# Kernel optimization log

Hardware: AMD Instinct MI355X
Metric: run time of the kernel (lower is better)

## Reference

```python
import jax, jax.numpy as jnp
import numpy as np

N = 100000   # nodes
R = 4        # relations
E = 200000   # edges per relation
IN = 256
HID = 64
OUT = 64
H = 8        # heads
NEG_SLOPE = 0.2


def setup_inputs() -> dict:
    key = jax.random.key(0)
    ks = jax.random.split(key, 13)
    s = 0.05
    return {
        "x": jax.random.normal(ks[0], (N, IN), jnp.float32),
        "src": jax.random.randint(ks[1], (R, E), 0, N),
        "dst": jax.random.randint(ks[2], (R, E), 0, N),
        "W0": jax.random.normal(ks[3], (R, IN, H * HID), jnp.float32) * s,
        "al0": jax.random.normal(ks[4], (R, H, HID), jnp.float32) * s,
        "ar0": jax.random.normal(ks[5], (R, H, HID), jnp.float32) * s,
        "W1": jax.random.normal(ks[6], (R, H * HID, H * HID), jnp.float32) * s,
        "al1": jax.random.normal(ks[7], (R, H, HID), jnp.float32) * s,
        "ar1": jax.random.normal(ks[8], (R, H, HID), jnp.float32) * s,
        "W2": jax.random.normal(ks[9], (R, H * HID, H * OUT), jnp.float32) * s,
        "al2": jax.random.normal(ks[10], (R, H, OUT), jnp.float32) * s,
        "ar2": jax.random.normal(ks[11], (R, H, OUT), jnp.float32) * s,
    }


def gat_layer(h, src, dst, W, al, ar):
    """Multi-relation GATConv layer; HeteroGraphConv sums ELU'd per-relation outputs.
    h: [N, in]; W: [R, in, H*O]; al/ar: [R, H, O]. Returns [N, H, O]."""
    n = h.shape[0]
    nheads, odim = al.shape[1], al.shape[2]
    acc = jnp.zeros((n, nheads, odim), h.dtype)
    for r in range(W.shape[0]):  # small fixed relation count
        f = (h @ W[r]).reshape(n, nheads, odim)          # [N,H,O]
        el = jnp.sum(f * al[r], axis=-1)                  # [N,H]
        er = jnp.sum(f * ar[r], axis=-1)                  # [N,H]
        s_r, d_r = src[r], dst[r]
        e = jax.nn.leaky_relu(el[s_r] + er[d_r], NEG_SLOPE)  # [E,H]
        # segment softmax over incoming edges per destination node
        m = jax.ops.segment_max(e, d_r, num_segments=n)
        m = jnp.where(jnp.isfinite(m), m, 0.0)
        ex = jnp.exp(e - m[d_r])
        denom = jax.ops.segment_sum(ex, d_r, num_segments=n)
        alpha = ex / (denom[d_r] + 1e-9)                  # [E,H]
        msg = f[s_r] * alpha[:, :, None]                  # [E,H,O]
        out_r = jax.ops.segment_sum(msg, d_r, num_segments=n)  # [N,H,O]
        acc = acc + jax.nn.elu(out_r)
    return acc


def reference(x, src, dst, W0, al0, ar0, W1, al1, ar1, W2, al2, ar2):
    h = gat_layer(x, src, dst, W0, al0, ar0).reshape(N, -1)   # flatten heads
    h = gat_layer(h, src, dst, W1, al1, ar1).reshape(N, -1)   # flatten heads
    h = gat_layer(h, src, dst, W2, al2, ar2).mean(axis=1)     # mean over heads
    return h
```

## Files before the change

### kernel.cpp

```cpp
#include <hip/hip_runtime.h>
#include <hip/hip_bf16.h>
#include <math.h>

#define NNODES 100000
#define NREL 4
#define NEDGE 200000
#define NH 8
#define FDIM 512
#define NMB 782

typedef float f4 __attribute__((ext_vector_type(4)));
typedef __bf16 bf16x8 __attribute__((ext_vector_type(8)));
typedef __bf16 bf16x4 __attribute__((ext_vector_type(4)));

__device__ __forceinline__ float eluf(float v) { return v > 0.f ? v : expm1f(v); }
__device__ __forceinline__ void gload16(const __bf16* g, __bf16* l) {
  __builtin_amdgcn_global_load_lds((const __attribute__((address_space(1))) void*)g,
                                   (__attribute__((address_space(3))) void*)l, 16, 0, 0);
}

__global__ void k_conv(const float* __restrict__ in, __bf16* __restrict__ outp) {
  int i = (blockIdx.x * 256 + threadIdx.x) * 4;
  f4 v = *(const f4*)(in + i);
  bf16x4 o = {(__bf16)v.x, (__bf16)v.y, (__bf16)v.z, (__bf16)v.w};
  *(bf16x4*)(outp + i) = o;
}
__global__ void k_copyb(const __bf16* __restrict__ in, __bf16* __restrict__ outp) {
  int i = (blockIdx.x * 256 + threadIdx.x) * 8;
  *(bf16x8*)(outp + i) = *(const bf16x8*)(in + i);
}

__global__ void k_transW(const float* __restrict__ W, __bf16* __restrict__ Wt, int K) {
  __shared__ float tile[32][33];
  int r = blockIdx.z;
  const float* Wr = W + (size_t)r * K * FDIM;
  __bf16* Wtr = Wt + (size_t)r * FDIM * K;
  int k0 = blockIdx.x * 32, n0 = blockIdx.y * 32;
  int tx = threadIdx.x, ty = threadIdx.y;
  for (int i = ty; i < 32; i += 8)
    tile[i][tx] = Wr[(size_t)(k0 + i) * FDIM + n0 + tx];
  __syncthreads();
  for (int i = ty; i < 32; i += 8)
    Wtr[(size_t)(n0 + i) * K + k0 + tx] = (__bf16)tile[tx][i];
}

__global__ __launch_bounds__(256) void k_gemm(const __bf16* __restrict__ A,
                                              const __bf16* __restrict__ BT,
                                              __bf16* __restrict__ C,
                                              const float* __restrict__ al,
                                              const float* __restrict__ ar,
                                              float* __restrict__ el,
                                              float* __restrict__ er, int M, int K,
                                              int nb4shift, int cpx) {
  __shared__ alignas(16) __bf16 lA[3][128 * 32];
  __shared__ alignas(16) __bf16 lB[3][128 * 32];
  int t = threadIdx.x, l = t & 63, w = t >> 6;
  int bid = blockIdx.x;
  int swz = (bid & 7) * cpx + (bid >> 3);
  int nb4mask = (1 << nb4shift) - 1;
  int m0 = (swz >> nb4shift) * 128, n0 = (swz & nb4mask) * 128;
  int NDIM = 128 << nb4shift;
  int nh_tot = 2 << nb4shift;
  int wm = (w >> 1) * 64, wn = (w & 1) * 64;
  f4 acc[4][4] = {};
  int r0 = t >> 2, c0 = t & 3;
  int ra = m0 + r0;      if (ra >= M) ra = M - 1;
  int rb = m0 + r0 + 64; if (rb >= M) rb = M - 1;
  const __bf16* gA0 = A + (size_t)ra * K + c0 * 8;
  const __bf16* gA1 = A + (size_t)rb * K + c0 * 8;
  const __bf16* gB0 = BT + (size_t)(n0 + r0) * K + c0 * 8;
  const __bf16* gB1 = BT + (size_t)(n0 + r0 + 64) * K + c0 * 8;

#define STAGE(buf, kk)                              \
  do {                                              \
    gload16(gA0 + (kk), &lA[buf][t * 8]);           \
    gload16(gA1 + (kk), &lA[buf][(t + 256) * 8]);   \
    gload16(gB0 + (kk), &lB[buf][t * 8]);           \
    gload16(gB1 + (kk), &lB[buf][(t + 256) * 8]);   \
  } while (0)

  int nt = K >> 5;
  STAGE(0, 0);
  STAGE(1, 32);
  STAGE(2, 64);
  int cur = 0;
  for (int kt = 0; kt < nt; kt++) {
    int rem = nt - 1 - kt;
    if (rem >= 2)      asm volatile("s_waitcnt vmcnt(8)" ::: "memory");
    else if (rem == 1) asm volatile("s_waitcnt vmcnt(4)" ::: "memory");
    else               asm volatile("s_waitcnt vmcnt(0)" ::: "memory");
    __builtin_amdgcn_s_barrier();
    bf16x8 a[4], b[4];
#pragma unroll
    for (int i = 0; i < 4; i++) {
      a[i] = *(const bf16x8*)(&lA[cur][(wm + i * 16 + (l & 15)) * 32 + (l >> 4) * 8]);
      b[i] = *(const bf16x8*)(&lB[cur][(wn + i * 16 + (l & 15)) * 32 + (l >> 4) * 8]);
    }
    asm volatile("s_waitcnt lgkmcnt(0)" ::: "memory");
    __builtin_amdgcn_s_barrier();
    if (kt + 3 < nt) STAGE(cur, (kt + 3) * 32);
#pragma unroll
    for (int i = 0; i < 4; i++)
#pragma unroll
      for (int j = 0; j < 4; j++)
        acc[i][j] = __builtin_amdgcn_mfma_f32_16x16x32_bf16(a[i], b[j], acc[i][j], 0, 0, 0);
    cur = (cur == 2) ? 0 : cur + 1;
  }
#undef STAGE

  int cn = n0 + wn + (l & 15);
  int rbase = m0 + wm + (l >> 4) * 4;
#pragma unroll
  for (int i = 0; i < 4; i++)
#pragma unroll
    for (int j = 0; j < 4; j++)
#pragma unroll
      for (int q = 0; q < 4; q++) {
        int row = rbase + i * 16 + q;
        if (row < M) C[(size_t)row * NDIM + cn + j * 16] = (__bf16)acc[i][j][q];
      }

  int h = (n0 + wn) >> 6;
  float av[4], bv[4];
#pragma unroll
  for (int j = 0; j < 4; j++) {
    av[j] = al[h * 64 + j * 16 + (l & 15)];
    bv[j] = ar[h * 64 + j * 16 + (l & 15)];
  }
#pragma unroll
  for (int i = 0; i < 4; i++)
#pragma unroll
    for (int q = 0; q < 4; q++) {
      float se = acc[i][0][q] * av[0] + acc[i][1][q] * av[1] +
                 acc[i][2][q] * av[2] + acc[i][3][q] * av[3];
      float sr = acc[i][0][q] * bv[0] + acc[i][1][q] * bv[1] +
                 acc[i][2][q] * bv[2] + acc[i][3][q] * bv[3];
      se += __shfl_xor(se, 1); se += __shfl_xor(se, 2);
      se += __shfl_xor(se, 4); se += __shfl_xor(se, 8);
      sr += __shfl_xor(sr, 1); sr += __shfl_xor(sr, 2);
      sr += __shfl_xor(sr, 4); sr += __shfl_xor(sr, 8);
      if ((l & 15) == 0) {
        int row = rbase + i * 16 + q;
        if (row < M) { el[row * nh_tot + h] = se; er[row * nh_tot + h] = sr; }
      }
    }
}

__global__ void k_count(const int* __restrict__ dst, int* __restrict__ deg) {
  int e = blockIdx.x * 256 + threadIdx.x;
  int r = blockIdx.y;
  if (e < NEDGE) {
    int d = dst[(size_t)r * NEDGE + e];
    if ((unsigned)d < (unsigned)NNODES) atomicAdd(&deg[r * NNODES + d], 1);
  }
}

__global__ __launch_bounds__(256) void k_scan_a(const int* __restrict__ in, int* __restrict__ out,
                                                int* __restrict__ bsum, int n) {
  __shared__ int wsums[4];
  int t = threadIdx.x, lane = t & 63, w = t >> 6;
  int base = blockIdx.x * 1024 + t * 4;
  int v0 = base + 0 < n ? in[base + 0] : 0;
  int v1 = base + 1 < n ? in[base + 1] : 0;
  int v2 = base + 2 < n ? in[base + 2] : 0;
  int v3 = base + 3 < n ? in[base + 3] : 0;
  int tot = v0 + v1 + v2 + v3;
  int sc = tot;
#pragma unroll
  for (int off = 1; off < 64; off <<= 1) {
    int u = __shfl_up(sc, off);
    if (lane >= off) sc += u;
  }
  if (lane == 63) wsums[w] = sc;
  __syncthreads();
  int add = 0;
#pragma unroll
  for (int i = 0; i < 4; i++)
    if (i < w) add += wsums[i];
  int excl = add + sc - tot;
  if (base + 0 < n) out[base + 0] = excl;
  if (base + 1 < n) out[base + 1] = excl + v0;
  if (base + 2 < n) out[base + 2] = excl + v0 + v1;
  if (base + 3 < n) out[base + 3] = excl + v0 + v1 + v2;
  if (t == 255) bsum[blockIdx.x] = add + sc;
}

__global__ __launch_bounds__(256) void k_scan_b(int* __restrict__ bsum, int nb) {
  __shared__ int wsums[4];
  int t = threadIdx.x, lane = t & 63, w = t >> 6;
  int i0 = t * 2, i1 = t * 2 + 1;
  int v0 = i0 < nb ? bsum[i0] : 0;
  int v1 = i1 < nb ? bsum[i1] : 0;
  int tot = v0 + v1, sc = tot;
#pragma unroll
  for (int off = 1; off < 64; off <<= 1) {
    int u = __shfl_up(sc, off);
    if (lane >= off) sc += u;
  }
  if (lane == 63) wsums[w] = sc;
  __syncthreads();
  int add = 0;
#pragma unroll
  for (int i = 0; i < 4; i++)
    if (i < w) add += wsums[i];
  int excl = add + sc - tot;
  if (i0 < nb) bsum[i0] = excl;
  if (i1 < nb) bsum[i1] = excl + v0;
}

__global__ void k_scan_c(int* __restrict__ out, const int* __restrict__ bsum, int n) {
  int i = blockIdx.x * 256 + threadIdx.x;
  if (i < n) out[i] += bsum[i >> 10];
}

__global__ void k_scatter(const int* __restrict__ src, const int* __restrict__ dst,
                          const int* __restrict__ ptrf, int* __restrict__ cur,
                          int* __restrict__ csrc) {
  int e = blockIdx.x * 256 + threadIdx.x;
  int r = blockIdx.y;
  if (e >= NEDGE) return;
  int d = dst[(size_t)r * NEDGE + e];
  if ((unsigned)d >= (unsigned)NNODES) return;
  int slot = ptrf[r * NNODES + d] + atomicAdd(&cur[r * NNODES + d], 1);
  if ((unsigned)slot < (unsigned)(NREL * NEDGE))
    csrc[slot] = src[(size_t)r * NEDGE + e];
}

__global__ void k_agg(const __bf16* __restrict__ f, const float* __restrict__ el,
                      const float* __restrict__ er, const int* __restrict__ ptrf,
                      const int* __restrict__ deg, const int* __restrict__ csrc,
                      __bf16* __restrict__ accG, int fstride, int coff, int estride, int eoff) {
  int t = threadIdx.x;
  int l = t & 63;
  int d = blockIdx.x * 4 + (t >> 6);
  int cnt = deg[d];
  if (cnt <= 0) return;
  int start = ptrf[d];
  if (start < 0) start = 0;
  if (start > NREL * NEDGE) start = NREL * NEDGE;
  if (cnt > NREL * NEDGE - start) cnt = NREL * NEDGE - start;
  int h = l >> 3;
  float erh = er[d * estride + eoff + h];
  float a[8] = {0.f, 0.f, 0.f, 0.f, 0.f, 0.f, 0.f, 0.f};
  float den = 0.f;
  for (int j = 0; j < cnt; j++) {
    int s = csrc[start + j];
    if ((unsigned)s >= (unsigned)NNODES) s = 0;
    float e = el[s * estride + eoff + h] + erh;
    e = (e > 0.f) ? e : 0.2f * e;
    float ex = __expf(e);
    den += ex;
    bf16x8 fv = *(const bf16x8*)(f + (size_t)s * fstride + coff + l * 8);
#pragma unroll
    for (int i = 0; i < 8; i++) a[i] += ex * (float)fv[i];
  }
  float inv = 1.f / (den + 1e-9f);
  __bf16* ap = accG + (size_t)d * FDIM + l * 8;
  bf16x8 cv = *(bf16x8*)ap;
  bf16x8 o;
#pragma unroll
  for (int i = 0; i < 8; i++) o[i] = (__bf16)((float)cv[i] + eluf(a[i] * inv));
  *(bf16x8*)ap = o;
}

__global__ void k_mean(const __bf16* __restrict__ acc, float* __restrict__ out) {
  int t = blockIdx.x * 256 + threadIdx.x;
  int n = t >> 6, o = t & 63;
  const __bf16* ap = acc + (size_t)n * FDIM + o;
  float s = 0.f;
#pragma unroll
  for (int h = 0; h < 8; h++) s += (float)ap[h * 64];
  out[t] = s * 0.125f;
}

extern "C" void kernel_launch(void* const* d_in, const int* in_sizes, int n_in,
                              void* d_out, int out_size, void* d_ws, size_t ws_size,
                              hipStream_t stream) {
  const float* x = (const float*)d_in[0];
  const int* srcp = (const int*)d_in[1];
  const int* dstp = (const int*)d_in[2];
  const float* Wl[3]  = {(const float*)d_in[3], (const float*)d_in[6], (const float*)d_in[9]};
  const float* alp[3] = {(const float*)d_in[4], (const float*)d_in[7], (const float*)d_in[10]};
  const float* arl[3] = {(const float*)d_in[5], (const float*)d_in[8], (const float*)d_in[11]};
  float* out = (float*)d_out;
  (void)in_sizes; (void)n_in; (void)out_size;

  auto rup = [](size_t b) { return (b + 255) & ~(size_t)255; };
  size_t sz_hin  = rup((size_t)NNODES * FDIM * 2);
  size_t sz_acc  = rup((size_t)NNODES * FDIM * 2);
  size_t sz_Wt   = rup((size_t)NREL * FDIM * FDIM * 2);
  size_t sz_int  = rup((size_t)NREL * NNODES * 4);
  size_t sz_csrc = rup((size_t)NREL * NEDGE * 4);
  size_t base_need = sz_hin + sz_acc + sz_Wt + 3 * sz_int + sz_csrc + rup(4096);
  size_t need_big   = base_need + rup((size_t)NNODES * 2048 * 2) + 2 * rup((size_t)NNODES * 32 * 4);
  size_t need_small = base_need + rup((size_t)NNODES * 512 * 2)  + 2 * rup((size_t)NNODES * 8 * 4);
  bool big;
  if (ws_size >= need_big) big = true;
  else if (ws_size >= need_small) big = false;
  else return;

  int nb = big ? 4 : 1;
  int nb4shift = big ? 4 : 2;
  int ncols = nb * FDIM;
  int nheads = nb * NH;

  char* ws = (char*)d_ws;
  size_t off = 0;
  auto alloc = [&](size_t bytes) -> void* { void* p = ws + off; off += rup(bytes); return p; };
  __bf16* hin  = (__bf16*)alloc((size_t)NNODES * FDIM * 2);
  __bf16* accG = (__bf16*)alloc((size_t)NNODES * FDIM * 2);
  __bf16* fbuf = (__bf16*)alloc((size_t)NNODES * ncols * 2);
  float* el    = (float*)alloc((size_t)NNODES * nheads * 4);
  float* er    = (float*)alloc((size_t)NNODES * nheads * 4);
  __bf16* Wt   = (__bf16*)alloc((size_t)NREL * FDIM * FDIM * 2);
  int* deg  = (int*)alloc((size_t)NREL * NNODES * 4);
  int* ptrf = (int*)alloc((size_t)NREL * NNODES * 4);
  int* cur  = (int*)alloc((size_t)NREL * NNODES * 4);
  int* csrc = (int*)alloc((size_t)NREL * NEDGE * 4);
  int* bsum = (int*)alloc(4096);

  hipMemsetAsync(deg, 0, (size_t)NREL * NNODES * 4, stream);
  hipMemsetAsync(cur, 0, (size_t)NREL * NNODES * 4, stream);
  k_count<<<dim3((NEDGE + 255) / 256, NREL), 256, 0, stream>>>(dstp, deg);
  int ntot = NREL * NNODES;
  int nb1 = (ntot + 1023) / 1024;
  k_scan_a<<<nb1, 256, 0, stream>>>(deg, ptrf, bsum, ntot);
  k_scan_b<<<1, 256, 0, stream>>>(bsum, nb1);
  k_scan_c<<<(ntot + 255) / 256, 256, 0, stream>>>(ptrf, bsum, ntot);
  k_scatter<<<dim3((NEDGE + 255) / 256, NREL), 256, 0, stream>>>(srcp, dstp, ptrf, cur, csrc);

  for (int L = 0; L < 3; L++) {
    int K = (L == 0) ? 256 : FDIM;
    if (L == 0) k_conv<<<(NNODES * 256) / 1024, 256, 0, stream>>>(x, hin);
    else        k_copyb<<<(NNODES * 512) / 2048, 256, 0, stream>>>(accG, hin);
    k_transW<<<dim3(K / 32, 16, NREL), dim3(32, 8), 0, stream>>>(Wl[L], Wt, K);
    hipMemsetAsync(accG, 0, (size_t)NNODES * FDIM * 2, stream);
    int ngrid = NMB * 4 * nb;
    int cpx = ngrid / 8;
    for (int g = 0; g < NREL / nb; g++) {
      k_gemm<<<ngrid, 256, 0, stream>>>(hin, Wt + (size_t)g * nb * FDIM * K, fbuf,
                                        alp[L] + g * nb * 512, arl[L] + g * nb * 512,
                                        el, er, NNODES, K, nb4shift, cpx);
      for (int q = 0; q < nb; q++) {
        int r = g * nb + q;
        k_agg<<<NNODES / 4, 256, 0, stream>>>(fbuf, el, er, ptrf + r * NNODES,
                                              deg + r * NNODES, csrc, accG,
                                              ncols, q * FDIM, nheads, q * NH);
      }
    }
  }
  k_mean<<<(NNODES * 64) / 256, 256, 0, stream>>>(accG, out);
}
```

Before: 2.222 ms.

## Widen GEMM tiles to 128x256, fuse relation aggregation, ping-pong layer buffers

The GEMM tile grows to 128x256 with double buffering instead of triple, an XOR-swizzled LDS layout and launch bounds of 2, to raise reuse and cut LDS bank conflicts. The relation batch drops from 4 to 2 relations per GEMM. One aggregation kernel now handles both relations per node, so the bf16 accumulator is read and written once per batch instead of once per relation. Ping-pong buffers replace the per-layer copy kernel. The wider tile raises register pressure, and the smaller batch means more GEMM launches.

```diff
diff --git a/kernel.cpp b/kernel.cpp
--- a/kernel.cpp
+++ b/kernel.cpp
@@ -24,10 +24,6 @@
   f4 v = *(const f4*)(in + i);
   bf16x4 o = {(__bf16)v.x, (__bf16)v.y, (__bf16)v.z, (__bf16)v.w};
   *(bf16x4*)(outp + i) = o;
-}
-__global__ void k_copyb(const __bf16* __restrict__ in, __bf16* __restrict__ outp) {
-  int i = (blockIdx.x * 256 + threadIdx.x) * 8;
-  *(bf16x8*)(outp + i) = *(const bf16x8*)(in + i);
 }
 
 __global__ void k_transW(const float* __restrict__ W, __bf16* __restrict__ Wt, int K) {
@@ -44,67 +40,75 @@
     Wtr[(size_t)(n0 + i) * K + k0 + tx] = (__bf16)tile[tx][i];
 }
 
-__global__ __launch_bounds__(256) void k_gemm(const __bf16* __restrict__ A,
-                                              const __bf16* __restrict__ BT,
-                                              __bf16* __restrict__ C,
-                                              const float* __restrict__ al,
-                                              const float* __restrict__ ar,
-                                              float* __restrict__ el,
-                                              float* __restrict__ er, int M, int K,
-                                              int nb4shift, int cpx) {
-  __shared__ alignas(16) __bf16 lA[3][128 * 32];
-  __shared__ alignas(16) __bf16 lB[3][128 * 32];
+__global__ __launch_bounds__(256, 2) void k_gemm(const __bf16* __restrict__ A,
+                                                 const __bf16* __restrict__ BT,
+                                                 __bf16* __restrict__ C,
+                                                 const float* __restrict__ al,
+                                                 const float* __restrict__ ar,
+                                                 float* __restrict__ el,
+                                                 float* __restrict__ er, int M, int K,
+                                                 int nnbsh) {
+  __shared__ alignas(16) __bf16 lA[2][128 * 32];
+  __shared__ alignas(16) __bf16 lB[2][256 * 32];
   int t = threadIdx.x, l = t & 63, w = t >> 6;
-  int bid = blockIdx.x;
-  int swz = (bid & 7) * cpx + (bid >> 3);
-  int nb4mask = (1 << nb4shift) - 1;
-  int m0 = (swz >> nb4shift) * 128, n0 = (swz & nb4mask) * 128;
-  int NDIM = 128 << nb4shift;
-  int nh_tot = 2 << nb4shift;
-  int wm = (w >> 1) * 64, wn = (w & 1) * 64;
-  f4 acc[4][4] = {};
-  int r0 = t >> 2, c0 = t & 3;
-  int ra = m0 + r0;      if (ra >= M) ra = M - 1;
-  int rb = m0 + r0 + 64; if (rb >= M) rb = M - 1;
-  const __bf16* gA0 = A + (size_t)ra * K + c0 * 8;
-  const __bf16* gA1 = A + (size_t)rb * K + c0 * 8;
-  const __bf16* gB0 = BT + (size_t)(n0 + r0) * K + c0 * 8;
-  const __bf16* gB1 = BT + (size_t)(n0 + r0 + 64) * K + c0 * 8;
-
-#define STAGE(buf, kk)                              \
-  do {                                              \
-    gload16(gA0 + (kk), &lA[buf][t * 8]);           \
-    gload16(gA1 + (kk), &lA[buf][(t + 256) * 8]);   \
-    gload16(gB0 + (kk), &lB[buf][t * 8]);           \
-    gload16(gB1 + (kk), &lB[buf][(t + 256) * 8]);   \
+  int nwg = gridDim.x, q = nwg >> 3, r8 = nwg & 7;
+  int x = blockIdx.x & 7, loc = blockIdx.x >> 3;
+  int swz = (x < r8 ? x * (q + 1) : r8 * (q + 1) + (x - r8) * q) + loc;
+  int nnbm = (1 << nnbsh) - 1;
+  int m0 = (swz >> nnbsh) * 128, n0 = (swz & nnbm) * 256;
+  int NDIM = 256 << nnbsh;
+  int nh_tot = 4 << nnbsh;
+  int wm = (w >> 1) * 64, wn = (w & 1) * 128;
+  f4 acc[4][8] = {};
+
+  const __bf16* pA[2];
+  const __bf16* pB[4];
+#pragma unroll
+  for (int u = 0; u < 2; u++) {
+    int s = t + u * 256;
+    int row = m0 + (s >> 2); if (row >= M) row = M - 1;
+    pA[u] = A + (size_t)row * K + (((s & 3) ^ ((s >> 2) & 3)) * 8);
+  }
+#pragma unroll
+  for (int u = 0; u < 4; u++) {
+    int s = t + u * 256;
+    pB[u] = BT + (size_t)(n0 + (s >> 2)) * K + (((s & 3) ^ ((s >> 2) & 3)) * 8);
+  }
+
+#define STAGE(buf, kk)                                      \
+  do {                                                      \
+    gload16(pA[0] + (kk), &lA[buf][t * 8]);                 \
+    gload16(pA[1] + (kk), &lA[buf][(t + 256) * 8]);         \
+    gload16(pB[0] + (kk), &lB[buf][t * 8]);                 \
+    gload16(pB[1] + (kk), &lB[buf][(t + 256) * 8]);         \
+    gload16(pB[2] + (kk), &lB[buf][(t + 512) * 8]);         \
+    gload16(pB[3] + (kk), &lB[buf][(t + 768) * 8]);         \
   } while (0)
 
   int nt = K >> 5;
   STAGE(0, 0);
   STAGE(1, 32);
-  STAGE(2, 64);
-  int cur = 0;
+  int segoff = ((l >> 4) ^ (l & 3)) * 8;
+  int rofA = (wm + (l & 15)) * 32 + segoff;
+  int rofB = (wn + (l & 15)) * 32 + segoff;
   for (int kt = 0; kt < nt; kt++) {
-    int rem = nt - 1 - kt;
-    if (rem >= 2)      asm volatile("s_waitcnt vmcnt(8)" ::: "memory");
-    else if (rem == 1) asm volatile("s_waitcnt vmcnt(4)" ::: "memory");
-    else               asm volatile("s_waitcnt vmcnt(0)" ::: "memory");
+    int cur = kt & 1;
+    if (kt + 1 < nt) asm volatile("s_waitcnt vmcnt(6)" ::: "memory");
+    else             asm volatile("s_waitcnt vmcnt(0)" ::: "memory");
     __builtin_amdgcn_s_barrier();
-    bf16x8 a[4], b[4];
-#pragma unroll
-    for (int i = 0; i < 4; i++) {
-      a[i] = *(const bf16x8*)(&lA[cur][(wm + i * 16 + (l & 15)) * 32 + (l >> 4) * 8]);
-      b[i] = *(const bf16x8*)(&lB[cur][(wn + i * 16 + (l & 15)) * 32 + (l >> 4) * 8]);
-    }
+    bf16x8 a[4], b[8];
+#pragma unroll
+    for (int i = 0; i < 4; i++) a[i] = *(const bf16x8*)(&lA[cur][rofA + i * 512]);
+#pragma unroll
+    for (int j = 0; j < 8; j++) b[j] = *(const bf16x8*)(&lB[cur][rofB + j * 512]);
     asm volatile("s_waitcnt lgkmcnt(0)" ::: "memory");
     __builtin_amdgcn_s_barrier();
-    if (kt + 3 < nt) STAGE(cur, (kt + 3) * 32);
+    if (kt + 2 < nt) STAGE(cur, (kt + 2) * 32);
 #pragma unroll
     for (int i = 0; i < 4; i++)
 #pragma unroll
-      for (int j = 0; j < 4; j++)
+      for (int j = 0; j < 8; j++)
         acc[i][j] = __builtin_amdgcn_mfma_f32_16x16x32_bf16(a[i], b[j], acc[i][j], 0, 0, 0);
-    cur = (cur == 2) ? 0 : cur + 1;
   }
 #undef STAGE
 
@@ -113,35 +117,49 @@
 #pragma unroll
   for (int i = 0; i < 4; i++)
 #pragma unroll
-    for (int j = 0; j < 4; j++)
-#pragma unroll
-      for (int q = 0; q < 4; q++) {
-        int row = rbase + i * 16 + q;
-        if (row < M) C[(size_t)row * NDIM + cn + j * 16] = (__bf16)acc[i][j][q];
+    for (int q2 = 0; q2 < 4; q2++) {
+      int row = rbase + i * 16 + q2;
+      if (row < M) {
+#pragma unroll
+        for (int j = 0; j < 8; j++)
+          C[(size_t)row * NDIM + cn + j * 16] = (__bf16)acc[i][j][q2];
       }
-
-  int h = (n0 + wn) >> 6;
-  float av[4], bv[4];
-#pragma unroll
-  for (int j = 0; j < 4; j++) {
-    av[j] = al[h * 64 + j * 16 + (l & 15)];
-    bv[j] = ar[h * 64 + j * 16 + (l & 15)];
+    }
+
+  int hbase = (n0 + wn) >> 6;
+  float av[8], bv[8];
+#pragma unroll
+  for (int j = 0; j < 8; j++) {
+    int h = hbase + (j >> 2);
+    av[j] = al[h * 64 + (j & 3) * 16 + (l & 15)];
+    bv[j] = ar[h * 64 + (j & 3) * 16 + (l & 15)];
   }
 #pragma unroll
   for (int i = 0; i < 4; i++)
 #pragma unroll
-    for (int q = 0; q < 4; q++) {
-      float se = acc[i][0][q] * av[0] + acc[i][1][q] * av[1] +
-                 acc[i][2][q] * av[2] + acc[i][3][q] * av[3];
-      float sr = acc[i][0][q] * bv[0] + acc[i][1][q] * bv[1] +
-                 acc[i][2][q] * bv[2] + acc[i][3][q] * bv[3];
-      se += __shfl_xor(se, 1); se += __shfl_xor(se, 2);
-      se += __shfl_xor(se, 4); se += __shfl_xor(se, 8);
-      sr += __shfl_xor(sr, 1); sr += __shfl_xor(sr, 2);
-      sr += __shfl_xor(sr, 4); sr += __shfl_xor(sr, 8);
-      if ((l & 15) == 0) {
-        int row = rbase + i * 16 + q;
-        if (row < M) { el[row * nh_tot + h] = se; er[row * nh_tot + h] = sr; }
+    for (int q2 = 0; q2 < 4; q2++) {
+#pragma unroll
+      for (int half = 0; half < 2; half++) {
+        float se = acc[i][half * 4 + 0][q2] * av[half * 4 + 0] +
+                   acc[i][half * 4 + 1][q2] * av[half * 4 + 1] +
+                   acc[i][half * 4 + 2][q2] * av[half * 4 + 2] +
+                   acc[i][half * 4 + 3][q2] * av[half * 4 + 3];
+        float sr = acc[i][half * 4 + 0][q2] * bv[half * 4 + 0] +
+                   acc[i][half * 4 + 1][q2] * bv[half * 4 + 1] +
+                   acc[i][half * 4 + 2][q2] * bv[half * 4 + 2] +
+                   acc[i][half * 4 + 3][q2] * bv[half * 4 + 3];
+        se += __shfl_xor(se, 1); se += __shfl_xor(se, 2);
+        se += __shfl_xor(se, 4); se += __shfl_xor(se, 8);
+        sr += __shfl_xor(sr, 1); sr += __shfl_xor(sr, 2);
+        sr += __shfl_xor(sr, 4); sr += __shfl_xor(sr, 8);
+        if ((l & 15) == 0) {
+          int row = rbase + i * 16 + q2;
+          if (row < M) {
+            int h = hbase + half;
+            el[row * nh_tot + h] = se;
+            er[row * nh_tot + h] = sr;
+          }
+        }
       }
     }
 }
@@ -229,37 +247,47 @@
 __global__ void k_agg(const __bf16* __restrict__ f, const float* __restrict__ el,
                       const float* __restrict__ er, const int* __restrict__ ptrf,
                       const int* __restrict__ deg, const int* __restrict__ csrc,
-                      __bf16* __restrict__ accG, int fstride, int coff, int estride, int eoff) {
+                      __bf16* __restrict__ accG, int fstride, int estride, int nrr) {
   int t = threadIdx.x;
   int l = t & 63;
   int d = blockIdx.x * 4 + (t >> 6);
-  int cnt = deg[d];
-  if (cnt <= 0) return;
-  int start = ptrf[d];
-  if (start < 0) start = 0;
-  if (start > NREL * NEDGE) start = NREL * NEDGE;
-  if (cnt > NREL * NEDGE - start) cnt = NREL * NEDGE - start;
   int h = l >> 3;
-  float erh = er[d * estride + eoff + h];
-  float a[8] = {0.f, 0.f, 0.f, 0.f, 0.f, 0.f, 0.f, 0.f};
-  float den = 0.f;
-  for (int j = 0; j < cnt; j++) {
-    int s = csrc[start + j];
-    if ((unsigned)s >= (unsigned)NNODES) s = 0;
-    float e = el[s * estride + eoff + h] + erh;
-    e = (e > 0.f) ? e : 0.2f * e;
-    float ex = __expf(e);
-    den += ex;
-    bf16x8 fv = *(const bf16x8*)(f + (size_t)s * fstride + coff + l * 8);
-#pragma unroll
-    for (int i = 0; i < 8; i++) a[i] += ex * (float)fv[i];
-  }
-  float inv = 1.f / (den + 1e-9f);
+  float res[8] = {0.f, 0.f, 0.f, 0.f, 0.f, 0.f, 0.f, 0.f};
+  bool touched = false;
+  for (int rr = 0; rr < nrr; rr++) {
+    int cnt = deg[rr * NNODES + d];
+    if (cnt <= 0) continue;
+    touched = true;
+    int start = ptrf[rr * NNODES + d];
+    if (start < 0) start = 0;
+    if (start > NREL * NEDGE) start = NREL * NEDGE;
+    if (cnt > NREL * NEDGE - start) cnt = NREL * NEDGE - start;
+    int eoff = rr * NH + h;
+    int coff = rr * FDIM + l * 8;
+    float erh = er[d * estride + eoff];
+    float a[8] = {0.f, 0.f, 0.f, 0.f, 0.f, 0.f, 0.f, 0.f};
+    float den = 0.f;
+    for (int j = 0; j < cnt; j++) {
+      int s = csrc[start + j];
+      if ((unsigned)s >= (unsigned)NNODES) s = 0;
+      float e = el[s * estride + eoff] + erh;
+      e = (e > 0.f) ? e : 0.2f * e;
+      float ex = __expf(e);
+      den += ex;
+      bf16x8 fv = *(const bf16x8*)(f + (size_t)s * fstride + coff);
+#pragma unroll
+      for (int i = 0; i < 8; i++) a[i] += ex * (float)fv[i];
+    }
+    float inv = 1.f / (den + 1e-9f);
+#pragma unroll
+    for (int i = 0; i < 8; i++) res[i] += eluf(a[i] * inv);
+  }
+  if (!touched) return;
   __bf16* ap = accG + (size_t)d * FDIM + l * 8;
   bf16x8 cv = *(bf16x8*)ap;
   bf16x8 o;
 #pragma unroll
-  for (int i = 0; i < 8; i++) o[i] = (__bf16)((float)cv[i] + eluf(a[i] * inv));
+  for (int i = 0; i < 8; i++) o[i] = (__bf16)((float)cv[i] + res[i]);
   *(bf16x8*)ap = o;
 }
 
@@ -286,30 +314,28 @@
   (void)in_sizes; (void)n_in; (void)out_size;
 
   auto rup = [](size_t b) { return (b + 255) & ~(size_t)255; };
-  size_t sz_hin  = rup((size_t)NNODES * FDIM * 2);
-  size_t sz_acc  = rup((size_t)NNODES * FDIM * 2);
+  size_t sz_buf  = rup((size_t)NNODES * FDIM * 2);
   size_t sz_Wt   = rup((size_t)NREL * FDIM * FDIM * 2);
   size_t sz_int  = rup((size_t)NREL * NNODES * 4);
   size_t sz_csrc = rup((size_t)NREL * NEDGE * 4);
-  size_t base_need = sz_hin + sz_acc + sz_Wt + 3 * sz_int + sz_csrc + rup(4096);
-  size_t need_big   = base_need + rup((size_t)NNODES * 2048 * 2) + 2 * rup((size_t)NNODES * 32 * 4);
-  size_t need_small = base_need + rup((size_t)NNODES * 512 * 2)  + 2 * rup((size_t)NNODES * 8 * 4);
-  bool big;
-  if (ws_size >= need_big) big = true;
-  else if (ws_size >= need_small) big = false;
+  size_t fixed = 2 * sz_buf + sz_Wt + 3 * sz_int + sz_csrc + rup(4096);
+  size_t need2 = fixed + rup((size_t)NNODES * 1024 * 2) + 2 * rup((size_t)NNODES * 16 * 4);
+  size_t need1 = fixed + rup((size_t)NNODES * 512 * 2)  + 2 * rup((size_t)NNODES * 8 * 4);
+  int nb;
+  if (ws_size >= need2) nb = 2;
+  else if (ws_size >= need1) nb = 1;
   else return;
 
-  int nb = big ? 4 : 1;
-  int nb4shift = big ? 4 : 2;
-  int ncols = nb * FDIM;
+  int NDIM = nb * FDIM;
   int nheads = nb * NH;
+  int nnbsh = (nb == 2) ? 2 : 1;
 
   char* ws = (char*)d_ws;
   size_t off = 0;
   auto alloc = [&](size_t bytes) -> void* { void* p = ws + off; off += rup(bytes); return p; };
-  __bf16* hin  = (__bf16*)alloc((size_t)NNODES * FDIM * 2);
-  __bf16* accG = (__bf16*)alloc((size_t)NNODES * FDIM * 2);
-  __bf16* fbuf = (__bf16*)alloc((size_t)NNODES * ncols * 2);
+  __bf16* bufA = (__bf16*)alloc((size_t)NNODES * FDIM * 2);
+  __bf16* bufB = (__bf16*)alloc((size_t)NNODES * FDIM * 2);
+  __bf16* fbuf = (__bf16*)alloc((size_t)NNODES * NDIM * 2);
   float* el    = (float*)alloc((size_t)NNODES * nheads * 4);
   float* er    = (float*)alloc((size_t)NNODES * nheads * 4);
   __bf16* Wt   = (__bf16*)alloc((size_t)NREL * FDIM * FDIM * 2);
@@ -329,25 +355,25 @@
   k_scan_c<<<(ntot + 255) / 256, 256, 0, stream>>>(ptrf, bsum, ntot);
   k_scatter<<<dim3((NEDGE + 255) / 256, NREL), 256, 0, stream>>>(srcp, dstp, ptrf, cur, csrc);
 
+  k_conv<<<(NNODES * 256) / 1024, 256, 0, stream>>>(x, bufA);
+
+  __bf16* inb = bufA;
+  __bf16* outb = bufB;
   for (int L = 0; L < 3; L++) {
     int K = (L == 0) ? 256 : FDIM;
-    if (L == 0) k_conv<<<(NNODES * 256) / 1024, 256, 0, stream>>>(x, hin);
-    else        k_copyb<<<(NNODES * 512) / 2048, 256, 0, stream>>>(accG, hin);
     k_transW<<<dim3(K / 32, 16, NREL), dim3(32, 8), 0, stream>>>(Wl[L], Wt, K);
-    hipMemsetAsync(accG, 0, (size_t)NNODES * FDIM * 2, stream);
-    int ngrid = NMB * 4 * nb;
-    int cpx = ngrid / 8;
+    hipMemsetAsync(outb, 0, (size_t)NNODES * FDIM * 2, stream);
+    int ngrid = NMB * (NDIM / 256);
     for (int g = 0; g < NREL / nb; g++) {
-      k_gemm<<<ngrid, 256, 0, stream>>>(hin, Wt + (size_t)g * nb * FDIM * K, fbuf,
-                                        alp[L] + g * nb * 512, arl[L] + g * nb * 512,
-                                        el, er, NNODES, K, nb4shift, cpx);
-      for (int q = 0; q < nb; q++) {
-        int r = g * nb + q;
-        k_agg<<<NNODES / 4, 256, 0, stream>>>(fbuf, el, er, ptrf + r * NNODES,
-                                              deg + r * NNODES, csrc, accG,
-                                              ncols, q * FDIM, nheads, q * NH);
-      }
+      k_gemm<<<ngrid, 256, 0, stream>>>(inb, Wt + (size_t)g * nb * FDIM * K, fbuf,
+                                        alp[L] + (size_t)g * nb * 512,
+                                        arl[L] + (size_t)g * nb * 512,
+                                        el, er, NNODES, K, nnbsh);
+      k_agg<<<NNODES / 4, 256, 0, stream>>>(fbuf, el, er, ptrf + (size_t)g * nb * NNODES,
+                                            deg + (size_t)g * nb * NNODES, csrc, outb,
+                                            NDIM, nheads, nb);
     }
-  }
-  k_mean<<<(NNODES * 64) / 256, 256, 0, stream>>>(accG, out);
-}
+    __bf16* tmp = inb; inb = outb; outb = tmp;
+  }
+  k_mean<<<(NNODES * 64) / 256, 256, 0, stream>>>(inb, out);
+}
```

After: 2.210 ms. No clear change (-0.5%).
